# Performance work log

Hardware: AMD Instinct MI355X
Metric: run time of the kernel (lower is better)

The kernel has to match this reference:

```python
import jax, jax.numpy as jnp
import numpy as np

B, C, H, W = 8, 32, 256, 256


def setup_inputs() -> dict:
    key = jax.random.key(0)
    k1, k2, k3, k4 = jax.random.split(key, 4)
    shape = (B, C, H, W)
    x = jax.random.normal(k1, shape, dtype=jnp.float32)
    G1 = jax.random.normal(k2, shape, dtype=jnp.float32)
    G2 = jax.random.normal(k3, shape, dtype=jnp.float32)
    G3 = jax.random.normal(k4, shape, dtype=jnp.float32)
    return {"x": x, "G1": G1, "G2": G2, "G3": G3}


def _spn_forward(x, G1, G2, G3):
    # --- SpnBlock gate normalization (elementwise) ---
    sum_abs = jnp.abs(G1) + jnp.abs(G2) + jnp.abs(G3)
    sum_abs = jnp.where(sum_abs == 0, jnp.asarray(1e-6, x.dtype), sum_abs)
    mask = (sum_abs >= 1).astype(x.dtype)  # only normalize where sum(|g|) >= 1
    keep = 1.0 - mask
    G1 = keep * G1 + mask * (G1 / sum_abs)
    G2 = keep * G2 + mask * (G2 / sum_abs)
    G3 = keep * G3 + mask * (G3 / sum_abs)

    # --- GateRecurrent2dnoind (horizontal=True, reverse=False): left->right scan ---
    # h[i,j] = (1 - g1 - g2 - g3) * x[i,j] + g1*h[i-1,j-1] + g2*h[i,j-1] + g3*h[i+1,j-1]
    # Gates whose neighbor is out of range are zeroed (CUDA kernel semantics).
    Hd, Wd = x.shape[2], x.shape[3]
    row = jnp.arange(Hd)
    col_ok = (jnp.arange(Wd) > 0).astype(x.dtype)[None, None, None, :]  # no left col at j=0
    up_ok = (row > 0).astype(x.dtype)[None, None, :, None]
    dn_ok = (row < Hd - 1).astype(x.dtype)[None, None, :, None]
    g1 = G1 * col_ok * up_ok
    g2 = G2 * col_ok
    g3 = G3 * col_ok * dn_ok

    # move scan axis (W) to front: [W, B, C, H]
    xs = jnp.moveaxis(x, 3, 0)
    g1s = jnp.moveaxis(g1, 3, 0)
    g2s = jnp.moveaxis(g2, 3, 0)
    g3s = jnp.moveaxis(g3, 3, 0)

    def step(h_prev, inp):
        xj, a, b, c = inp  # each [B, C, H]
        zero = jnp.zeros_like(h_prev[..., :1])
        up = jnp.concatenate([zero, h_prev[..., :-1]], axis=-1)   # h_prev at row i-1
        dn = jnp.concatenate([h_prev[..., 1:], zero], axis=-1)    # h_prev at row i+1
        h = (1.0 - a - b - c) * xj + a * up + b * h_prev + c * dn
        return h, h

    init = jnp.zeros(x.shape[:3], dtype=x.dtype)  # [B, C, H]
    _, hs = jax.lax.scan(step, init, (xs, g1s, g2s, g3s))
    return jnp.moveaxis(hs, 0, 3)  # back to [B, C, H, W]


def reference(x, G1, G2, G3):
    return _spn_forward(x, G1, G2, G3)
```

## Files before the change

kernel.cpp:

```cpp
#include <hip/hip_runtime.h>


#define HD 256
#define WD 256
#define NS 32
#define STG 260
#define ARR_F (8 * STG)
#define STAGE_F (4 * ARR_F)
#define TILE_OFF (3 * STAGE_F)

#define F4E(v, e) ((e) == 0 ? (v).x : (e) == 1 ? (v).y : (e) == 2 ? (v).z : (v).w)

#define FENCE_BAR()                                      \
  do {                                                   \
    asm volatile("s_waitcnt lgkmcnt(0)" ::: "memory");   \
    __builtin_amdgcn_s_barrier();                        \
    asm volatile("" ::: "memory");                       \
  } while (0)

__global__ __launch_bounds__(320, 1) void spn_fwd(
    const float* __restrict__ x, const float* __restrict__ G1,
    const float* __restrict__ G2, const float* __restrict__ G3,
    float* __restrict__ out)
{
  __shared__ float lds_f[3 * STAGE_F + 16 * STG];

  const int tid = threadIdx.x;
  const int wid = tid >> 6;
  const int l   = tid & 63;
  const size_t pbase = (size_t)blockIdx.x * (HD * WD);
  const float* gp[4] = {x + pbase, G1 + pbase, G2 + pbase, G3 + pbase};
  float* op = out + pbase;

  if (wid < 4) {
    const int rq = l >> 2;
    const int cq = l & 3;
    const int myhalf = cq >> 1;
    float4 R[4][4];

    auto issueBlk = [&](int k) {
#pragma unroll
      for (int A = 0; A < 4; ++A)
#pragma unroll
        for (int i = 0; i < 4; ++i)
          R[A][i] = *(const float4*)(gp[A] +
              (size_t)(64 * wid + 16 * i + rq) * WD + 16 * k + 4 * cq);
    };

    auto normBlk = [&](int k) {
#pragma unroll
      for (int i = 0; i < 4; ++i) {
        const int row = 64 * wid + 16 * i + rq;
        const float uOk = (row > 0) ? 1.f : 0.f;
        const float dOk = (row < HD - 1) ? 1.f : 0.f;
        float nx[4], na[4], nb[4], nc[4];
#pragma unroll
        for (int e = 0; e < 4; ++e) {
          float a = F4E(R[1][i], e), b = F4E(R[2][i], e), c = F4E(R[3][i], e);
          float xx = F4E(R[0][i], e);
          float s = fabsf(a) + fabsf(b) + fabsf(c);
          float inv = (s >= 1.f) ? __builtin_amdgcn_rcpf(s) : 1.f;
          float cOk = (16 * k + 4 * cq + e > 0) ? 1.f : 0.f;
          float ga = a * inv * cOk * uOk;
          float gb = b * inv * cOk;
          float gc = c * inv * cOk * dOk;
          nx[e] = (1.f - ga - gb - gc) * xx;
          na[e] = ga; nb[e] = gb; nc[e] = gc;
        }
        R[0][i] = make_float4(nx[0], nx[1], nx[2], nx[3]);
        R[1][i] = make_float4(na[0], na[1], na[2], na[3]);
        R[2][i] = make_float4(nb[0], nb[1], nb[2], nb[3]);
        R[3][i] = make_float4(nc[0], nc[1], nc[2], nc[3]);
      }
    };

    auto writeHalf = [&](int hf, float* dst) {
      if (myhalf == hf) {
        const int c0 = 4 * cq - 8 * hf;
#pragma unroll
        for (int A = 0; A < 4; ++A)
#pragma unroll
          for (int i = 0; i < 4; ++i) {
            const int row = 64 * wid + 16 * i + rq;
#pragma unroll
            for (int e = 0; e < 4; ++e)
              dst[A * ARR_F + (c0 + e) * STG + row] = F4E(R[A][i], e);
          }
      }
    };

    issueBlk(0);
    normBlk(0);
    writeHalf(0, lds_f + 0 * STAGE_F);
    writeHalf(1, lds_f + 1 * STAGE_F);
    issueBlk(1);
    FENCE_BAR();

#pragma unroll 1
    for (int t = 0; t < NS; ++t) {
      if (t + 2 < NS) {
        float* dst = lds_f + ((t + 2) % 3) * STAGE_F;
        if ((t & 1) == 0) {
          normBlk((t + 2) >> 1);
          writeHalf(0, dst);
        } else {
          writeHalf(1, dst);
          if (t <= 27) issueBlk((t + 3) >> 1);
        }
      }
      FENCE_BAR();
    }
  } else {
    __builtin_amdgcn_s_setprio(1);
    float h[4] = {0.f, 0.f, 0.f, 0.f};
    const int cb = 4 * (l & 3);
    const int rr = l >> 2;
    float* tile = lds_f + TILE_OFF;

    FENCE_BAR();

#pragma unroll 1
    for (int t = 0; t < NS; ++t) {
      const float* src = lds_f + (t % 3) * STAGE_F;
      float* tl = tile + (t & 1) * (8 * STG);
#pragma unroll
      for (int c = 0; c < 8; ++c) {
        float4 d4 = *(const float4*)(src + 0 * ARR_F + c * STG + 4 * l);
        float4 a4 = *(const float4*)(src + 1 * ARR_F + c * STG + 4 * l);
        float4 b4 = *(const float4*)(src + 2 * ARR_F + c * STG + 4 * l);
        float4 c4 = *(const float4*)(src + 3 * ARR_F + c * STG + 4 * l);
        const float shU = __shfl_up(h[3], 1);
        const float shD = __shfl_down(h[0], 1);
        float hn[4];
#pragma unroll
        for (int r = 0; r < 4; ++r) {
          float up = (r == 0) ? shU : h[r - 1];
          float dn = (r == 3) ? shD : h[r + 1];
          hn[r] = fmaf(F4E(a4, r), up,
                  fmaf(F4E(b4, r), h[r],
                  fmaf(F4E(c4, r), dn, F4E(d4, r))));
        }
#pragma unroll
        for (int r = 0; r < 4; ++r) h[r] = hn[r];
        *(float4*)(tl + c * STG + 4 * l) = make_float4(hn[0], hn[1], hn[2], hn[3]);
      }
      if (t & 1) {
        const int jc = 16 * (t >> 1);
#pragma unroll
        for (int kk = 0; kk < 16; ++kk) {
          const int row = 16 * kk + rr;
          float4 o;
          o.x = tile[(cb + 0) * STG + row];
          o.y = tile[(cb + 1) * STG + row];
          o.z = tile[(cb + 2) * STG + row];
          o.w = tile[(cb + 3) * STG + row];
          *(float4*)(op + (size_t)row * WD + jc + cb) = o;
        }
      }
      FENCE_BAR();
    }
  }
}

extern "C" void kernel_launch(void* const* d_in, const int* in_sizes, int n_in,
                              void* d_out, int out_size, void* d_ws, size_t ws_size,
                              hipStream_t stream) {
  const float* x  = (const float*)d_in[0];
  const float* g1 = (const float*)d_in[1];
  const float* g2 = (const float*)d_in[2];
  const float* g3 = (const float*)d_in[3];
  float* outp = (float*)d_out;
  const int planes = out_size / (HD * WD);
  spn_fwd<<<planes, 320, 0, stream>>>(x, g1, g2, g3, outp);
}
```

Before: 100.5 us.

## Double-buffer producer register blocks to prefetch two column blocks ahead

Producer waves now hold two register sets (RA/RB) so global loads for a block are issued two blocks ahead instead of one, giving each load more barrier intervals to complete before normalization. Both producer and consumer loops are unrolled by four steps so the buffer alternation is static. This is meant to hide global memory latency on the producer side of the scan. In exchange it doubles producer register use (64 more VGPRs per lane) and makes the code larger.

```diff
diff --git a/kernel.cpp b/kernel.cpp
--- a/kernel.cpp
+++ b/kernel.cpp
@@ -36,9 +36,9 @@
     const int rq = l >> 2;
     const int cq = l & 3;
     const int myhalf = cq >> 1;
-    float4 R[4][4];
+    float4 RA[4][4], RB[4][4];
 
-    auto issueBlk = [&](int k) {
+    auto issueBlk = [&](float4 (&R)[4][4], int k) {
 #pragma unroll
       for (int A = 0; A < 4; ++A)
 #pragma unroll
@@ -47,7 +47,7 @@
               (size_t)(64 * wid + 16 * i + rq) * WD + 16 * k + 4 * cq);
     };
 
-    auto normBlk = [&](int k) {
+    auto normBlk = [&](float4 (&R)[4][4], int k) {
 #pragma unroll
       for (int i = 0; i < 4; ++i) {
         const int row = 64 * wid + 16 * i + rq;
@@ -74,7 +74,7 @@
       }
     };
 
-    auto writeHalf = [&](int hf, float* dst) {
+    auto writeHalf = [&](float4 (&R)[4][4], int hf, float* dst) {
       if (myhalf == hf) {
         const int c0 = 4 * cq - 8 * hf;
 #pragma unroll
@@ -89,25 +89,31 @@
       }
     };
 
-    issueBlk(0);
-    normBlk(0);
-    writeHalf(0, lds_f + 0 * STAGE_F);
-    writeHalf(1, lds_f + 1 * STAGE_F);
-    issueBlk(1);
+    issueBlk(RA, 0);
+    issueBlk(RB, 1);
+    normBlk(RA, 0);
+    writeHalf(RA, 0, lds_f + 0 * STAGE_F);
+    writeHalf(RA, 1, lds_f + 1 * STAGE_F);
+    issueBlk(RA, 2);
     FENCE_BAR();
 
 #pragma unroll 1
-    for (int t = 0; t < NS; ++t) {
-      if (t + 2 < NS) {
-        float* dst = lds_f + ((t + 2) % 3) * STAGE_F;
-        if ((t & 1) == 0) {
-          normBlk((t + 2) >> 1);
-          writeHalf(0, dst);
-        } else {
-          writeHalf(1, dst);
-          if (t <= 27) issueBlk((t + 3) >> 1);
-        }
+    for (int tt = 0; tt < 8; ++tt) {
+      const int t0 = 4 * tt;
+      const int kb = t0 / 2;
+      normBlk(RB, kb + 1);
+      writeHalf(RB, 0, lds_f + ((t0 + 2) % 3) * STAGE_F);
+      FENCE_BAR();
+      writeHalf(RB, 1, lds_f + ((t0 + 3) % 3) * STAGE_F);
+      if (kb + 3 <= 15) issueBlk(RB, kb + 3);
+      FENCE_BAR();
+      if (kb + 2 <= 15) {
+        normBlk(RA, kb + 2);
+        writeHalf(RA, 0, lds_f + ((t0 + 4) % 3) * STAGE_F);
       }
+      FENCE_BAR();
+      if (kb + 2 <= 15) writeHalf(RA, 1, lds_f + ((t0 + 5) % 3) * STAGE_F);
+      if (kb + 4 <= 15) issueBlk(RA, kb + 4);
       FENCE_BAR();
     }
   } else {
@@ -117,10 +123,7 @@
     const int rr = l >> 2;
     float* tile = lds_f + TILE_OFF;
 
-    FENCE_BAR();
-
-#pragma unroll 1
-    for (int t = 0; t < NS; ++t) {
+    auto consume = [&](int t) {
       const float* src = lds_f + (t % 3) * STAGE_F;
       float* tl = tile + (t & 1) * (8 * STG);
 #pragma unroll
@@ -157,7 +160,17 @@
           *(float4*)(op + (size_t)row * WD + jc + cb) = o;
         }
       }
-      FENCE_BAR();
+    };
+
+    FENCE_BAR();
+
+#pragma unroll 1
+    for (int tt = 0; tt < 8; ++tt) {
+      const int t0 = 4 * tt;
+      consume(t0);     FENCE_BAR();
+      consume(t0 + 1); FENCE_BAR();
+      consume(t0 + 2); FENCE_BAR();
+      consume(t0 + 3); FENCE_BAR();
     }
   }
 }
```

Result: faster. 98.10 us (-2.4%).
